# Kernel tuning notes

Measured on AMD Instinct MI355X. Metric: run time of the kernel, lower is better.

Reference implementation:

```python
import jax, jax.numpy as jnp
import numpy as np

D_MODEL = 512
N_HEADS = 8
D_FF = 1024
LV = 2048
LT = 512
GAMMA = 0.9
SCALE_BASE = 512  # XPOS default scale_base


def _dup_interleave(m):
    # (L, d/2) -> (L, d) duplicating each column: [a,b] -> [a,a,b,b]
    return jnp.repeat(m, 2, axis=-1)


def _xpos(x, downscale=False):
    # XPOS rotary embedding (RetNet-style), x: (B, L, d)
    B, L, d = x.shape
    half = d // 2
    s = (jnp.arange(0, d, 2, dtype=jnp.float32) + 0.4 * d) / (1.4 * d)  # (d/2,)
    scale = s[None, :] ** (jnp.arange(L, dtype=jnp.float32)[:, None] / SCALE_BASE)  # (L, d/2)
    inv_freq = 1.0 / (10000.0 ** (jnp.arange(half, dtype=jnp.float32) / half))
    ang = jnp.arange(L, dtype=jnp.float32)[:, None] * inv_freq[None, :]  # (L, d/2)
    if downscale:
        scale = 1.0 / scale
    sin = _dup_interleave(jnp.sin(ang) * scale)[None]  # (1, L, d)
    cos = _dup_interleave(jnp.cos(ang) * scale)[None]
    x1, x2 = x[..., 0::2], x[..., 1::2]
    rot = jnp.stack((-x2, x1), axis=-1).reshape(x.shape)  # rotate_every_two
    return x * cos + rot * sin


def _sine_pos(L, d):
    # DETR-style normalized 1D sine position embedding, mask = ones(1, L)
    x_embed = jnp.arange(1, L + 1, dtype=jnp.float32)  # cumsum of ones
    x_embed = x_embed / (x_embed[-1] + 1e-6) * (2.0 * np.pi)
    dim_t = jnp.arange(d, dtype=jnp.float32)
    dim_t = 10000.0 ** (2.0 * jnp.floor(dim_t / 2.0) / d)
    pos = x_embed[:, None] / dim_t[None, :]  # (L, d)
    pos = jnp.stack((jnp.sin(pos[:, 0::2]), jnp.cos(pos[:, 1::2])), axis=2).reshape(L, d)
    return pos[None]  # (1, L, d)


def _ln(x, w, b, eps=1e-5):
    mu = jnp.mean(x, axis=-1, keepdims=True)
    var = jnp.var(x, axis=-1, keepdims=True)
    return (x - mu) / jnp.sqrt(var + eps) * w + b


def _ret_forward(src_vid, src_txt, ln1_w, ln1_b, wq, bq, wk, bk, wv, bv, wo, bo,
                 lin1_w, lin1_b, lin2_w, lin2_b, ln2_w, ln2_b, ln3_w, ln3_b,
                 learn_ret_w):
    B, Lv, D = src_vid.shape
    Lt = src_txt.shape[1]
    h, dk = N_HEADS, D // N_HEADS

    # retention decay matrix D[n,m] = gamma^(n-m) for n>=m else 0
    n = jnp.arange(Lv)
    delta = jnp.maximum(n[:, None] - n[None, :], 0).astype(jnp.float32)
    Dm = jnp.where(n[:, None] >= n[None, :], GAMMA ** delta, 0.0)

    # learned sparse mask
    learn = jax.nn.sigmoid(learn_ret_w.reshape(Lv, Lv))
    diag = jnp.eye(Lv, dtype=jnp.float32)
    video_ret = (1.0 - diag) * learn
    learn_mask = diag + video_ret
    mask = Dm * learn_mask  # mask_choice == 'both'
    loss_sparsity = jnp.mean(jnp.abs(video_ret))

    # position encodings
    pos_vid_q = _xpos(src_vid)
    pos_vid_k = _xpos(src_vid, downscale=True)
    pos_txt = _sine_pos(Lt, D)
    src = jnp.concatenate([src_vid, src_txt], axis=1)       # (B, Lv+Lt, D)
    pos = jnp.concatenate([pos_vid_q, pos_txt], axis=1)
    pos_k = jnp.concatenate([pos_vid_k, pos_txt], axis=1)

    # --- RetLayer (eval mode: dropout = identity) ---
    src2 = _ln(src, ln1_w, ln1_b)
    q = src2[:, :Lv] + pos[:, :Lv]
    k = src2[:, :Lv] + pos_k[:, :Lv]
    v = src2[:, :Lv]

    # multi-head attention with MULTIPLICATIVE mask on logits
    qh = (q @ wq.T + bq).reshape(B, Lv, h, dk) / jnp.sqrt(jnp.float32(dk))
    kh = (k @ wk.T + bk).reshape(B, Lv, h, dk)
    vh = (v @ wv.T + bv).reshape(B, Lv, h, dk)
    attn = jnp.einsum('blhd,bmhd->bhlm', qh, kh) * mask[None, None]
    attn = jax.nn.softmax(attn, axis=-1)
    vid_att = jnp.einsum('bhlm,bmhd->blhd', attn, vh).reshape(B, Lv, D)
    vid_att = vid_att @ wo.T + bo

    src2 = jnp.concatenate([vid_att, src2[:, Lv:]], axis=1) + pos
    src = src + src2
    src2 = _ln(src, ln2_w, ln2_b)
    src2 = jax.nn.gelu(src2 @ lin1_w.T + lin1_b, approximate=False) @ lin2_w.T + lin2_b
    src = src + src2
    src = _ln(src, ln3_w, ln3_b)
    return src[:, :Lv], src[:, Lv:], loss_sparsity


def setup_inputs() -> dict:
    key = jax.random.key(0)
    ks = jax.random.split(key, 12)
    D, F = D_MODEL, D_FF
    w = lambda k, shp: (jax.random.normal(k, shp, dtype=jnp.float32) * 0.02)
    return {
        'src_vid': jax.random.normal(ks[0], (1, LV, D), dtype=jnp.float32),
        'src_txt': jax.random.normal(ks[1], (1, LT, D), dtype=jnp.float32),
        'ln1_w': jnp.ones((D,), jnp.float32), 'ln1_b': jnp.zeros((D,), jnp.float32),
        'wq': w(ks[2], (D, D)), 'bq': jnp.zeros((D,), jnp.float32),
        'wk': w(ks[3], (D, D)), 'bk': jnp.zeros((D,), jnp.float32),
        'wv': w(ks[4], (D, D)), 'bv': jnp.zeros((D,), jnp.float32),
        'wo': w(ks[5], (D, D)), 'bo': jnp.zeros((D,), jnp.float32),
        'lin1_w': w(ks[6], (F, D)), 'lin1_b': jnp.zeros((F,), jnp.float32),
        'lin2_w': w(ks[7], (D, F)), 'lin2_b': jnp.zeros((D,), jnp.float32),
        'ln2_w': jnp.ones((D,), jnp.float32), 'ln2_b': jnp.zeros((D,), jnp.float32),
        'ln3_w': jnp.ones((D,), jnp.float32), 'ln3_b': jnp.zeros((D,), jnp.float32),
        'learn_ret_w': jax.random.normal(ks[8], (LV * LV,), dtype=jnp.float32),
    }


def reference(src_vid, src_txt, ln1_w, ln1_b, wq, bq, wk, bk, wv, bv, wo, bo,
              lin1_w, lin1_b, lin2_w, lin2_b, ln2_w, ln2_b, ln3_w, ln3_b,
              learn_ret_w):
    return _ret_forward(src_vid, src_txt, ln1_w, ln1_b, wq, bq, wk, bk, wv, bv,
                        wo, bo, lin1_w, lin1_b, lin2_w, lin2_b, ln2_w, ln2_b,
                        ln3_w, ln3_b, learn_ret_w)
```

## Files before the change

### kernel.cpp

```cpp
#include <hip/hip_runtime.h>
#include <hip/hip_bf16.h>
#include <math.h>

#define LVID 2048
#define LTXT 512
#define DMOD 512
#define LTOT 2560
#define LOG2_GAMMA (-0.15200309344504995f)
#define LOG2E 1.4426950408889634f

typedef __bf16 bf16x8 __attribute__((ext_vector_type(8)));
typedef float f32x4 __attribute__((ext_vector_type(4)));

__device__ inline f32x4 mfma_bf16(bf16x8 a, bf16x8 b, f32x4 c) {
  return __builtin_amdgcn_mfma_f32_16x16x32_bf16(a, b, c, 0, 0, 0);
}

__device__ inline void gload_lds16(const void* g, void* l) {
  __builtin_amdgcn_global_load_lds(
      (const __attribute__((address_space(1))) void*)g,
      (__attribute__((address_space(3))) void*)l, 16, 0, 0);
}

union U8 { __hip_bfloat16 b[8]; uint4 u; };

__global__ __launch_bounds__(256) void k_prep_ln1(
    const float* __restrict__ lw, float* __restrict__ premask2,
    float* __restrict__ lossp,
    const float* __restrict__ wq, const float* __restrict__ wk,
    const float* __restrict__ wv, const float* __restrict__ wo,
    const float* __restrict__ l1, const float* __restrict__ l2,
    __hip_bfloat16* __restrict__ dst,
    const float* __restrict__ src_vid, const float* __restrict__ src_txt,
    const float* __restrict__ w, const float* __restrict__ b,
    __hip_bfloat16* __restrict__ acat, float* __restrict__ srcA,
    float* __restrict__ posb) {
  int tid = threadIdx.x;
  int blk = blockIdx.x;
  if (blk < 2048) {
    __shared__ float red[256];
    int idx0 = (blk * 256 + tid) * 8;
    int i = idx0 >> 11, j0 = idx0 & 2047;
    float4 lv0 = *(const float4*)&lw[idx0];
    float4 lv1 = *(const float4*)&lw[idx0 + 4];
    float lvv[8] = {lv0.x, lv0.y, lv0.z, lv0.w, lv1.x, lv1.y, lv1.z, lv1.w};
    float pm[8];
    float s = 0.f;
#pragma unroll
    for (int e = 0; e < 8; e++) {
      int j = j0 + e;
      float sig = 1.f / (1.f + __expf(-lvv[e]));
      if (j != i) s += sig;
      float m = (j > i) ? 0.f
              : ((j == i) ? 1.f : exp2f((float)(i - j) * LOG2_GAMMA) * sig);
      pm[e] = m * LOG2E;
    }
    *(float4*)&premask2[idx0]     = *(float4*)&pm[0];
    *(float4*)&premask2[idx0 + 4] = *(float4*)&pm[4];
    red[tid] = s; __syncthreads();
    for (int st = 128; st > 0; st >>= 1) { if (tid < st) red[tid] += red[tid + st]; __syncthreads(); }
    if (tid == 0) lossp[blk] = red[0];
  } else if (blk < 4096) {
    int i4 = (blk - 2048) * 256 + tid;
    const float* sp; int base;
    if (i4 < 131072)      { if (i4 < 65536)  { sp = wq; base = 0; }      else { sp = wk; base = 65536; } }
    else if (i4 < 262144) { if (i4 < 196608) { sp = wv; base = 131072; } else { sp = wo; base = 196608; } }
    else if (i4 < 393216) { sp = l1; base = 262144; }
    else                  { sp = l2; base = 393216; }
    float4 v = ((const float4*)sp)[i4 - base];
    __hip_bfloat16 o[4] = {__float2bfloat16(v.x), __float2bfloat16(v.y),
                           __float2bfloat16(v.z), __float2bfloat16(v.w)};
    *(uint2*)(dst + (size_t)i4 * 4) = *(uint2*)o;
  } else {
    int row = (blk - 4096) * 4 + (tid >> 6);
    int lane = tid & 63;
    const float* xs = (row < LVID) ? (src_vid + (size_t)row * DMOD)
                                   : (src_txt + (size_t)(row - LVID) * DMOD);
    float x[8];
    { float4 v0 = *(const float4*)&xs[lane * 8];
      float4 v1 = *(const float4*)&xs[lane * 8 + 4];
      x[0]=v0.x; x[1]=v0.y; x[2]=v0.z; x[3]=v0.w;
      x[4]=v1.x; x[5]=v1.y; x[6]=v1.z; x[7]=v1.w; }
    float s = 0.f;
#pragma unroll
    for (int i = 0; i < 8; i++) s += x[i];
#pragma unroll
    for (int st = 1; st < 64; st <<= 1) s += __shfl_xor(s, st, 64);
    float mu = s * (1.f / DMOD);
    float vs = 0.f;
#pragma unroll
    for (int i = 0; i < 8; i++) { float d = x[i] - mu; vs += d * d; }
#pragma unroll
    for (int st = 1; st < 64; st <<= 1) vs += __shfl_xor(vs, st, 64);
    float inv = rsqrtf(vs * (1.f / DMOD) + 1e-5f);
    float y[8];
    { float4 w0 = *(const float4*)&w[lane * 8];
      float4 w1 = *(const float4*)&w[lane * 8 + 4];
      float4 b0 = *(const float4*)&b[lane * 8];
      float4 b1 = *(const float4*)&b[lane * 8 + 4];
      float wv_[8] = {w0.x,w0.y,w0.z,w0.w,w1.x,w1.y,w1.z,w1.w};
      float bv_[8] = {b0.x,b0.y,b0.z,b0.w,b1.x,b1.y,b1.z,b1.w};
#pragma unroll
      for (int i = 0; i < 8; i++) y[i] = (x[i] - mu) * inv * wv_[i] + bv_[i]; }
    size_t base = (size_t)row * DMOD + lane * 8;
    if (row < LVID) {
      U8 pv;
#pragma unroll
      for (int i = 0; i < 8; i++) pv.b[i] = __float2bfloat16(y[i]);
      *(uint4*)&acat[(size_t)(4096 + row) * DMOD + lane * 8] = pv.u;
      float pq[8], pk[8];
      float l = (float)row;
#pragma unroll
      for (int p = 0; p < 4; p++) {
        int j = lane * 4 + p;
        float sj = (2.f * j + 204.8f) * (1.f / 716.8f);
        float scale = __powf(sj, l * (1.f / 512.f));
        float invfreq = __powf(10000.f, -(float)j * (1.f / 256.f));
        float sn, cs; __sincosf(l * invfreq, &sn, &cs);
        float cq = cs * scale, sq = sn * scale;
        pq[2*p]   = x[2*p] * cq - x[2*p+1] * sq;
        pq[2*p+1] = x[2*p+1] * cq + x[2*p] * sq;
        float isc = 1.f / scale;
        float ck = cs * isc, sk = sn * isc;
        pk[2*p]   = x[2*p] * ck - x[2*p+1] * sk;
        pk[2*p+1] = x[2*p+1] * ck + x[2*p] * sk;
      }
      *(float4*)&posb[base]     = *(float4*)&pq[0];
      *(float4*)&posb[base + 4] = *(float4*)&pq[4];
      U8 pqv, pkv;
#pragma unroll
      for (int i = 0; i < 8; i++) {
        pqv.b[i] = __float2bfloat16(y[i] + pq[i]);
        pkv.b[i] = __float2bfloat16(y[i] + pk[i]);
      }
      *(uint4*)&acat[(size_t)row * DMOD + lane * 8] = pqv.u;
      *(uint4*)&acat[(size_t)(2048 + row) * DMOD + lane * 8] = pkv.u;
    } else {
      int l = row - LVID;
      float xe = (float)(l + 1) * (6.28318530717958647692f / 512.000001f);
      float o8[8];
#pragma unroll
      for (int p = 0; p < 4; p++) {
        int j = lane * 4 + p;
        float dimt = __powf(10000.f, (float)j * (1.f / 256.f));
        float a = xe / dimt;
        o8[2*p]   = x[2*p]   + y[2*p]   + __sinf(a);
        o8[2*p+1] = x[2*p+1] + y[2*p+1] + __cosf(a);
      }
      *(float4*)&srcA[base]     = *(float4*)&o8[0];
      *(float4*)&srcA[base + 4] = *(float4*)&o8[4];
    }
  }
}

__global__ __launch_bounds__(256) void k_ln2(
    const float* __restrict__ srcA,
    const float* __restrict__ w, const float* __restrict__ b,
    __hip_bfloat16* __restrict__ obf) {
  int row = blockIdx.x * 4 + (threadIdx.x >> 6);
  int lane = threadIdx.x & 63;
  size_t base = (size_t)row * DMOD + lane * 8;
  float x[8];
  { float4 v0 = *(const float4*)&srcA[base];
    float4 v1 = *(const float4*)&srcA[base + 4];
    x[0]=v0.x; x[1]=v0.y; x[2]=v0.z; x[3]=v0.w;
    x[4]=v1.x; x[5]=v1.y; x[6]=v1.z; x[7]=v1.w; }
  float s = 0.f;
#pragma unroll
  for (int i = 0; i < 8; i++) s += x[i];
#pragma unroll
  for (int st = 1; st < 64; st <<= 1) s += __shfl_xor(s, st, 64);
  float mu = s * (1.f / DMOD);
  float vs = 0.f;
#pragma unroll
  for (int i = 0; i < 8; i++) { float d = x[i] - mu; vs += d * d; }
#pragma unroll
  for (int st = 1; st < 64; st <<= 1) vs += __shfl_xor(vs, st, 64);
  float inv = rsqrtf(vs * (1.f / DMOD) + 1e-5f);
  float4 w0 = *(const float4*)&w[lane * 8];
  float4 w1 = *(const float4*)&w[lane * 8 + 4];
  float4 b0 = *(const float4*)&b[lane * 8];
  float4 b1 = *(const float4*)&b[lane * 8 + 4];
  float wv_[8] = {w0.x,w0.y,w0.z,w0.w,w1.x,w1.y,w1.z,w1.w};
  float bv_[8] = {b0.x,b0.y,b0.z,b0.w,b1.x,b1.y,b1.z,b1.w};
  U8 o;
#pragma unroll
  for (int i = 0; i < 8; i++)
    o.b[i] = __float2bfloat16((x[i] - mu) * inv * wv_[i] + bv_[i]);
  *(uint4*)&obf[base] = o.u;
}

__global__ __launch_bounds__(256) void k_ln3(
    const float* __restrict__ srcA, const float* __restrict__ ffo,
    const float* __restrict__ w, const float* __restrict__ b,
    float* __restrict__ o, const float* __restrict__ lossp) {
  if (blockIdx.x == 0 && threadIdx.x < 64) {
    float s = 0.f;
    for (int i = threadIdx.x; i < 2048; i += 64) s += lossp[i];
#pragma unroll
    for (int st = 1; st < 64; st <<= 1) s += __shfl_xor(s, st, 64);
    if (threadIdx.x == 0) o[1310720] = s * (1.f / 4194304.f);
  }
  int row = blockIdx.x * 4 + (threadIdx.x >> 6);
  int lane = threadIdx.x & 63;
  size_t base = (size_t)row * DMOD + lane * 8;
  float x[8];
  { float4 a0 = *(const float4*)&srcA[base];
    float4 a1 = *(const float4*)&srcA[base + 4];
    float4 f0 = *(const float4*)&ffo[base];
    float4 f1 = *(const float4*)&ffo[base + 4];
    x[0]=a0.x+f0.x; x[1]=a0.y+f0.y; x[2]=a0.z+f0.z; x[3]=a0.w+f0.w;
    x[4]=a1.x+f1.x; x[5]=a1.y+f1.y; x[6]=a1.z+f1.z; x[7]=a1.w+f1.w; }
  float s = 0.f;
#pragma unroll
  for (int i = 0; i < 8; i++) s += x[i];
#pragma unroll
  for (int st = 1; st < 64; st <<= 1) s += __shfl_xor(s, st, 64);
  float mu = s * (1.f / DMOD);
  float vs = 0.f;
#pragma unroll
  for (int i = 0; i < 8; i++) { float d = x[i] - mu; vs += d * d; }
#pragma unroll
  for (int st = 1; st < 64; st <<= 1) vs += __shfl_xor(vs, st, 64);
  float inv = rsqrtf(vs * (1.f / DMOD) + 1e-5f);
  float4 w0 = *(const float4*)&w[lane * 8];
  float4 w1 = *(const float4*)&w[lane * 8 + 4];
  float4 b0 = *(const float4*)&b[lane * 8];
  float4 b1 = *(const float4*)&b[lane * 8 + 4];
  float wv_[8] = {w0.x,w0.y,w0.z,w0.w,w1.x,w1.y,w1.z,w1.w};
  float bv_[8] = {b0.x,b0.y,b0.z,b0.w,b1.x,b1.y,b1.z,b1.w};
  float y[8];
#pragma unroll
  for (int i = 0; i < 8; i++) y[i] = (x[i] - mu) * inv * wv_[i] + bv_[i];
  *(float4*)&o[base]     = *(float4*)&y[0];
  *(float4*)&o[base + 4] = *(float4*)&y[4];
}

template <int EPI>
__global__ __launch_bounds__(256) void k_gemm3(
    const __hip_bfloat16* __restrict__ A, const __hip_bfloat16* __restrict__ W0,
    const float* __restrict__ b0, const float* __restrict__ b1,
    const float* __restrict__ b2, void* __restrict__ Cv,
    const float* __restrict__ res1, const float* __restrict__ res2,
    float* __restrict__ vtot, int M, int N, int K) {
  __shared__ __hip_bfloat16 sA[2][4096];
  __shared__ __hip_bfloat16 sB[2][4096];
  int tid = threadIdx.x, lane = tid & 63, w = tid >> 6;
  int c16 = lane & 15, q4 = lane >> 4;
  int bm = blockIdx.y * 128, bn = blockIdx.x * 128;
  int seg = (EPI == 3) ? (bm >> 11) : 0;
  const __hip_bfloat16* Wp = (EPI == 3) ? (W0 + (size_t)seg * ((size_t)N * K)) : W0;
  int r0 = tid >> 2, cc0 = (tid & 3) * 8;
  const __hip_bfloat16* gA0 = A  + (size_t)(bm + r0) * K + cc0;
  const __hip_bfloat16* gA1 = A  + (size_t)(bm + 64 + r0) * K + cc0;
  const __hip_bfloat16* gB0 = Wp + (size_t)(bn + r0) * K + cc0;
  const __hip_bfloat16* gB1 = Wp + (size_t)(bn + 64 + r0) * K + cc0;
  auto stage = [&](int buf, int k0) {
    gload_lds16(gA0 + k0, &sA[buf][(size_t)tid * 8]);
    gload_lds16(gA1 + k0, &sA[buf][2048 + (size_t)tid * 8]);
    gload_lds16(gB0 + k0, &sB[buf][(size_t)tid * 8]);
    gload_lds16(gB1 + k0, &sB[buf][2048 + (size_t)tid * 8]);
  };
  f32x4 acc[4][4];
  { f32x4 z = {0.f,0.f,0.f,0.f};
#pragma unroll
    for (int i = 0; i < 4; i++)
#pragma unroll
      for (int j = 0; j < 4; j++) acc[i][j] = z; }
  int wm = w & 1, wn = w >> 1;
  const int S = K >> 5;
  stage(0, 0);
  for (int s = 0; s < S; s++) {
    __syncthreads();
    if (s + 1 < S) stage((s + 1) & 1, (s + 1) * 32);
    int bf = s & 1;
    bf16x8 af[4], bfr[4];
#pragma unroll
    for (int i = 0; i < 4; i++)
      af[i] = *(const bf16x8*)&sA[bf][(wm*64 + i*16 + c16) * 32 + q4*8];
#pragma unroll
    for (int j = 0; j < 4; j++)
      bfr[j] = *(const bf16x8*)&sB[bf][(wn*64 + j*16 + c16) * 32 + q4*8];
#pragma unroll
    for (int i = 0; i < 4; i++)
#pragma unroll
      for (int j = 0; j < 4; j++)
        acc[i][j] = mfma_bf16(af[i], bfr[j], acc[i][j]);
  }
  float alpha = (EPI == 3 && seg == 0) ? 0.125f : 1.f;
  const float* bp = (EPI == 3) ? (seg == 0 ? b0 : (seg == 1 ? b1 : b2)) : b0;
  float vsum[4] = {0.f, 0.f, 0.f, 0.f};
#pragma unroll
  for (int j = 0; j < 4; j++) {
    int n = bn + wn*64 + j*16 + c16;
    float bs = bp[n];
#pragma unroll
    for (int i = 0; i < 4; i++) {
#pragma unroll
      for (int r = 0; r < 4; r++) {
        int m = bm + wm*64 + i*16 + q4*4 + r;
        float v = (acc[i][j][r] + bs) * alpha;
        if (EPI == 4) v = 0.5f * v * (1.f + erff(v * 0.70710678118654752f));
        if (EPI == 0) {
          ((float*)Cv)[(size_t)m * N + n] = v;
        } else if (EPI == 2) {
          size_t off = (size_t)m * N + n;
          ((float*)Cv)[off] = v + res1[off] + res2[off];
        } else if (EPI == 4) {
          ((__hip_bfloat16*)Cv)[(size_t)m * N + n] = __float2bfloat16(v);
        } else {
          __hip_bfloat16 vb = __float2bfloat16(v);
          ((__hip_bfloat16*)Cv)[(size_t)(m & 2047) * 1536 + seg * 512 + n] = vb;
          if (seg == 2) vsum[j] += __bfloat162float(vb);
        }
      }
    }
  }
  if (EPI == 3 && seg == 2) {
#pragma unroll
    for (int j = 0; j < 4; j++) {
      float s2 = vsum[j];
      s2 += __shfl_xor(s2, 16, 64);
      s2 += __shfl_xor(s2, 32, 64);
      if (q4 == 0) atomicAdd(&vtot[bn + wn*64 + j*16 + c16], s2);
    }
  }
}

__global__ __launch_bounds__(256) void k_attn(
    const __hip_bfloat16* __restrict__ qkv,
    const float* __restrict__ premask2,
    const float* __restrict__ Vtot,
    __hip_bfloat16* __restrict__ outp) {
  __shared__ __hip_bfloat16 sQ[64][72];
  __shared__ __hip_bfloat16 sK[2][64][72];
  __shared__ __hip_bfloat16 sVt[2][64][72];
  __shared__ __hip_bfloat16 sP[64][72];
  __shared__ float sVa[4][64];
  int i0 = blockIdx.x * 64, h = blockIdx.y;
  int tid = threadIdx.x, lane = tid & 63, w = tid >> 6;
  int c16 = lane & 15, q4 = lane >> 4;
  {
    int r = tid >> 2, c0 = (tid & 3) * 16;
    const __hip_bfloat16* g = qkv + (size_t)(i0 + r) * 1536 + h * 64 + c0;
    *(uint4*)&sQ[r][c0]     = *(const uint4*)g;
    *(uint4*)&sQ[r][c0 + 8] = *(const uint4*)(g + 8);
  }
  int thi = i0 >> 6;
  int tlo = (i0 > 900) ? ((i0 - 900) >> 6) : 0;
  float rm = 0.f, rz = 0.f;
  f32x4 O[4];
  { f32x4 z = {0.f,0.f,0.f,0.f}; O[0]=z; O[1]=z; O[2]=z; O[3]=z; }
  float vacc = 0.f;
  int kr = tid >> 2, kc = (tid & 3) * 16;
  uint4 pk0, pk1;
  U8 pv0, pv1;
  {
    const __hip_bfloat16* gk = qkv + (size_t)(tlo*64 + kr) * 1536 + 512 + h*64 + kc;
    pk0 = *(const uint4*)gk; pk1 = *(const uint4*)(gk + 8);
    const __hip_bfloat16* gv = qkv + (size_t)(tlo*64 + w*16) * 1536 + 1024 + h*64 + lane;
#pragma unroll
    for (int j = 0; j < 8; j++) pv0.b[j] = gv[(size_t)j * 1536];
#pragma unroll
    for (int j = 0; j < 8; j++) pv1.b[j] = gv[(size_t)(j + 8) * 1536];
  }
  for (int t = tlo; t <= thi; t++) {
    int buf = (t - tlo) & 1;
    *(uint4*)&sK[buf][kr][kc]       = pk0;
    *(uint4*)&sK[buf][kr][kc + 8]   = pk1;
    *(uint4*)&sVt[buf][lane][w*16]     = pv0.u;
    *(uint4*)&sVt[buf][lane][w*16 + 8] = pv1.u;
#pragma unroll
    for (int j = 0; j < 8; j++) vacc += __bfloat162float(pv0.b[j]);
#pragma unroll
    for (int j = 0; j < 8; j++) vacc += __bfloat162float(pv1.b[j]);
    __syncthreads();
    if (t < thi) {
      const __hip_bfloat16* gk = qkv + (size_t)((t+1)*64 + kr) * 1536 + 512 + h*64 + kc;
      pk0 = *(const uint4*)gk; pk1 = *(const uint4*)(gk + 8);
      const __hip_bfloat16* gv = qkv + (size_t)((t+1)*64 + w*16) * 1536 + 1024 + h*64 + lane;
#pragma unroll
      for (int j = 0; j < 8; j++) pv0.b[j] = gv[(size_t)j * 1536];
#pragma unroll
      for (int j = 0; j < 8; j++) pv1.b[j] = gv[(size_t)(j + 8) * 1536];
    }
    bf16x8 bq0 = *(const bf16x8*)&sQ[w*16 + c16][q4*8];
    bf16x8 bq1 = *(const bf16x8*)&sQ[w*16 + c16][32 + q4*8];
    f32x4 St[4];
#pragma unroll
    for (int jt = 0; jt < 4; jt++) {
      f32x4 z = {0.f,0.f,0.f,0.f};
      bf16x8 a0 = *(const bf16x8*)&sK[buf][jt*16 + c16][q4*8];
      bf16x8 a1 = *(const bf16x8*)&sK[buf][jt*16 + c16][32 + q4*8];
      z = mfma_bf16(a0, bq0, z);
      z = mfma_bf16(a1, bq1, z);
      St[jt] = z;
    }
    int qg = i0 + w*16 + c16;
    float lg[4][4];
    float tmax = -3.0e38f;
#pragma unroll
    for (int jt = 0; jt < 4; jt++) {
      float4 pm = *(const float4*)&premask2[(size_t)qg * 2048 + t*64 + jt*16 + q4*4];
      lg[jt][0] = St[jt][0] * pm.x; lg[jt][1] = St[jt][1] * pm.y;
      lg[jt][2] = St[jt][2] * pm.z; lg[jt][3] = St[jt][3] * pm.w;
#pragma unroll
      for (int r = 0; r < 4; r++) tmax = fmaxf(tmax, lg[jt][r]);
    }
    tmax = fmaxf(tmax, __shfl_xor(tmax, 16, 64));
    tmax = fmaxf(tmax, __shfl_xor(tmax, 32, 64));
    float mn = fmaxf(rm, tmax);
    float al = exp2f(rm - mn);
    rm = mn;
    float zp = 0.f;
#pragma unroll
    for (int jt = 0; jt < 4; jt++) {
      U8 e4;
      float e0 = exp2f(lg[jt][0] - rm), e1 = exp2f(lg[jt][1] - rm);
      float e2 = exp2f(lg[jt][2] - rm), e3 = exp2f(lg[jt][3] - rm);
      zp += e0 + e1 + e2 + e3;
      e4.b[0] = __float2bfloat16(e0); e4.b[1] = __float2bfloat16(e1);
      e4.b[2] = __float2bfloat16(e2); e4.b[3] = __float2bfloat16(e3);
      *(uint2*)&sP[w*16 + c16][jt*16 + q4*4] = *(uint2*)&e4.b[0];
    }
    zp += __shfl_xor(zp, 16, 64);
    zp += __shfl_xor(zp, 32, 64);
    rz = rz * al + zp;
    float alr[4];
#pragma unroll
    for (int r = 0; r < 4; r++) alr[r] = __shfl(al, q4*4 + r, 64);
#pragma unroll
    for (int dt = 0; dt < 4; dt++)
#pragma unroll
      for (int r = 0; r < 4; r++) O[dt][r] *= alr[r];
    bf16x8 ap0 = *(const bf16x8*)&sP[w*16 + c16][q4*8];
    bf16x8 ap1 = *(const bf16x8*)&sP[w*16 + c16][32 + q4*8];
#pragma unroll
    for (int dt = 0; dt < 4; dt++) {
      bf16x8 bv0 = *(const bf16x8*)&sVt[buf][dt*16 + c16][q4*8];
      bf16x8 bv1 = *(const bf16x8*)&sVt[buf][dt*16 + c16][32 + q4*8];
      O[dt] = mfma_bf16(ap0, bv0, O[dt]);
      O[dt] = mfma_bf16(ap1, bv1, O[dt]);
    }
  }
  sVa[w][lane] = vacc;
  __syncthreads();
  float rmr[4], rzr[4];
#pragma unroll
  for (int r = 0; r < 4; r++) {
    rmr[r] = __shfl(rm, q4*4 + r, 64);
    rzr[r] = __shfl(rz, q4*4 + r, 64);
  }
  float nu = (float)(2048 - 64 * (thi - tlo + 1));
#pragma unroll
  for (int dt = 0; dt < 4; dt++) {
    int d = dt*16 + c16;
    float va = sVa[0][d] + sVa[1][d] + sVa[2][d] + sVa[3][d];
    float vu = Vtot[h*64 + d] - va;
#pragma unroll
    for (int r = 0; r < 4; r++) {
      float eu = exp2f(-rmr[r]);
      float o = (O[dt][r] + eu * vu) / (rzr[r] + nu * eu);
      outp[(size_t)(i0 + w*16 + q4*4 + r) * DMOD + h*64 + d] = __float2bfloat16(o);
    }
  }
}

extern "C" void kernel_launch(void* const* d_in, const int* in_sizes, int n_in,
                              void* d_out, int out_size, void* d_ws, size_t ws_size,
                              hipStream_t stream) {
  const float* src_vid = (const float*)d_in[0];
  const float* src_txt = (const float*)d_in[1];
  const float* ln1_w = (const float*)d_in[2];
  const float* ln1_b = (const float*)d_in[3];
  const float* wq = (const float*)d_in[4];
  const float* bq = (const float*)d_in[5];
  const float* wk = (const float*)d_in[6];
  const float* bk = (const float*)d_in[7];
  const float* wv = (const float*)d_in[8];
  const float* bv = (const float*)d_in[9];
  const float* wo = (const float*)d_in[10];
  const float* bo = (const float*)d_in[11];
  const float* lin1_w = (const float*)d_in[12];
  const float* lin1_b = (const float*)d_in[13];
  const float* lin2_w = (const float*)d_in[14];
  const float* lin2_b = (const float*)d_in[15];
  const float* ln2_w = (const float*)d_in[16];
  const float* ln2_b = (const float*)d_in[17];
  const float* ln3_w = (const float*)d_in[18];
  const float* ln3_b = (const float*)d_in[19];
  const float* lw = (const float*)d_in[20];
  float* out = (float*)d_out;

  char* wsb = (char*)d_ws;
  float* premask2       = (float*)(wsb + 0);
  __hip_bfloat16* wqb   = (__hip_bfloat16*)(wsb + 16777216);
  __hip_bfloat16* wob   = wqb + 786432;
  __hip_bfloat16* l1b   = wqb + 1048576;
  __hip_bfloat16* l2b   = wqb + 1572864;
  __hip_bfloat16* acat  = (__hip_bfloat16*)(wsb + 20971520);
  __hip_bfloat16* qkvb  = (__hip_bfloat16*)(wsb + 27262976);
  __hip_bfloat16* vattb = (__hip_bfloat16*)(wsb + 33554432);
  float* srcA           = (float*)(wsb + 35651584);
  float* posb           = (float*)(wsb + 46137344);
  __hip_bfloat16* s2b   = (__hip_bfloat16*)(wsb + 51380224);
  __hip_bfloat16* hidb  = (__hip_bfloat16*)(wsb + 54525952);
  float* ffo            = (float*)(wsb + 59768832);
  float* Vtot           = (float*)(wsb + 65011712);
  float* lossp          = Vtot + 512;

  hipMemsetAsync(Vtot, 0, 512 * sizeof(float), stream);

  k_prep_ln1<<<4736, 256, 0, stream>>>(lw, premask2, lossp,
      wq, wk, wv, wo, lin1_w, lin2_w, wqb,
      src_vid, src_txt, ln1_w, ln1_b, acat, srcA, posb);

  k_gemm3<3><<<dim3(4, 48), 256, 0, stream>>>(acat, wqb, bq, bk, bv,
      qkvb, nullptr, nullptr, Vtot, 6144, 512, 512);
  k_attn<<<dim3(32, 8), 256, 0, stream>>>(qkvb, premask2, Vtot, vattb);
  k_gemm3<2><<<dim3(4, 16), 256, 0, stream>>>(vattb, wob, bo, nullptr, nullptr,
      srcA, src_vid, posb, nullptr, 2048, 512, 512);
  k_ln2<<<640, 256, 0, stream>>>(srcA, ln2_w, ln2_b, s2b);
  k_gemm3<4><<<dim3(8, 20), 256, 0, stream>>>(s2b, l1b, lin1_b, nullptr, nullptr,
      hidb, nullptr, nullptr, nullptr, 2560, 1024, 512);
  k_gemm3<0><<<dim3(4, 20), 256, 0, stream>>>(hidb, l2b, lin2_b, nullptr, nullptr,
      ffo, nullptr, nullptr, nullptr, 2560, 512, 1024);
  k_ln3<<<640, 256, 0, stream>>>(srcA, ffo, ln3_w, ln3_b, out, lossp);
}
```

Before: 245.7 us.

## Shrink GEMM tiles to 64x64 and split-K the second FFN GEMM

Every GEMM now uses 64x64 block tiles instead of 128x128, giving four times as many workgroups so the small matrices fill more of the GPU's compute units. The lin2 GEMM is also split along K into two halves that write separate fp32 partial buffers, and the LN3 kernel sums them. The cost is less data reuse per tile, more global and LDS traffic per flop, and an extra fp32 buffer that LN3 must read.

```diff
diff --git a/kernel.cpp b/kernel.cpp
--- a/kernel.cpp
+++ b/kernel.cpp
@@ -191,7 +191,8 @@
 }
 
 __global__ __launch_bounds__(256) void k_ln3(
-    const float* __restrict__ srcA, const float* __restrict__ ffo,
+    const float* __restrict__ srcA, const float* __restrict__ ffo0,
+    const float* __restrict__ ffo1,
     const float* __restrict__ w, const float* __restrict__ b,
     float* __restrict__ o, const float* __restrict__ lossp) {
   if (blockIdx.x == 0 && threadIdx.x < 64) {
@@ -207,10 +208,12 @@
   float x[8];
   { float4 a0 = *(const float4*)&srcA[base];
     float4 a1 = *(const float4*)&srcA[base + 4];
-    float4 f0 = *(const float4*)&ffo[base];
-    float4 f1 = *(const float4*)&ffo[base + 4];
-    x[0]=a0.x+f0.x; x[1]=a0.y+f0.y; x[2]=a0.z+f0.z; x[3]=a0.w+f0.w;
-    x[4]=a1.x+f1.x; x[5]=a1.y+f1.y; x[6]=a1.z+f1.z; x[7]=a1.w+f1.w; }
+    float4 f0 = *(const float4*)&ffo0[base];
+    float4 f1 = *(const float4*)&ffo0[base + 4];
+    float4 g0 = *(const float4*)&ffo1[base];
+    float4 g1 = *(const float4*)&ffo1[base + 4];
+    x[0]=a0.x+f0.x+g0.x; x[1]=a0.y+f0.y+g0.y; x[2]=a0.z+f0.z+g0.z; x[3]=a0.w+f0.w+g0.w;
+    x[4]=a1.x+f1.x+g1.x; x[5]=a1.y+f1.y+g1.y; x[6]=a1.z+f1.z+g1.z; x[7]=a1.w+f1.w+g1.w; }
   float s = 0.f;
 #pragma unroll
   for (int i = 0; i < 8; i++) s += x[i];
@@ -237,77 +240,69 @@
 }
 
 template <int EPI>
-__global__ __launch_bounds__(256) void k_gemm3(
+__global__ __launch_bounds__(256) void k_gemm4(
     const __hip_bfloat16* __restrict__ A, const __hip_bfloat16* __restrict__ W0,
     const float* __restrict__ b0, const float* __restrict__ b1,
     const float* __restrict__ b2, void* __restrict__ Cv,
     const float* __restrict__ res1, const float* __restrict__ res2,
     float* __restrict__ vtot, int M, int N, int K) {
-  __shared__ __hip_bfloat16 sA[2][4096];
-  __shared__ __hip_bfloat16 sB[2][4096];
+  __shared__ __hip_bfloat16 sA[2][2048];
+  __shared__ __hip_bfloat16 sB[2][2048];
   int tid = threadIdx.x, lane = tid & 63, w = tid >> 6;
   int c16 = lane & 15, q4 = lane >> 4;
-  int bm = blockIdx.y * 128, bn = blockIdx.x * 128;
+  int bm = blockIdx.y * 64, bn = blockIdx.x * 64;
   int seg = (EPI == 3) ? (bm >> 11) : 0;
   const __hip_bfloat16* Wp = (EPI == 3) ? (W0 + (size_t)seg * ((size_t)N * K)) : W0;
+  int kb   = (EPI == 5) ? (int)blockIdx.z * (K >> 1) : 0;
+  int Keff = (EPI == 5) ? (K >> 1) : K;
   int r0 = tid >> 2, cc0 = (tid & 3) * 8;
-  const __hip_bfloat16* gA0 = A  + (size_t)(bm + r0) * K + cc0;
-  const __hip_bfloat16* gA1 = A  + (size_t)(bm + 64 + r0) * K + cc0;
-  const __hip_bfloat16* gB0 = Wp + (size_t)(bn + r0) * K + cc0;
-  const __hip_bfloat16* gB1 = Wp + (size_t)(bn + 64 + r0) * K + cc0;
+  const __hip_bfloat16* gA = A  + (size_t)(bm + r0) * K + kb + cc0;
+  const __hip_bfloat16* gB = Wp + (size_t)(bn + r0) * K + kb + cc0;
   auto stage = [&](int buf, int k0) {
-    gload_lds16(gA0 + k0, &sA[buf][(size_t)tid * 8]);
-    gload_lds16(gA1 + k0, &sA[buf][2048 + (size_t)tid * 8]);
-    gload_lds16(gB0 + k0, &sB[buf][(size_t)tid * 8]);
-    gload_lds16(gB1 + k0, &sB[buf][2048 + (size_t)tid * 8]);
+    gload_lds16(gA + k0, &sA[buf][(size_t)tid * 8]);
+    gload_lds16(gB + k0, &sB[buf][(size_t)tid * 8]);
   };
-  f32x4 acc[4][4];
-  { f32x4 z = {0.f,0.f,0.f,0.f};
-#pragma unroll
-    for (int i = 0; i < 4; i++)
-#pragma unroll
-      for (int j = 0; j < 4; j++) acc[i][j] = z; }
+  f32x4 acc[2][2];
+  { f32x4 z = {0.f,0.f,0.f,0.f}; acc[0][0]=z; acc[0][1]=z; acc[1][0]=z; acc[1][1]=z; }
   int wm = w & 1, wn = w >> 1;
-  const int S = K >> 5;
+  const int S = Keff >> 5;
   stage(0, 0);
   for (int s = 0; s < S; s++) {
     __syncthreads();
     if (s + 1 < S) stage((s + 1) & 1, (s + 1) * 32);
     int bf = s & 1;
-    bf16x8 af[4], bfr[4];
-#pragma unroll
-    for (int i = 0; i < 4; i++)
-      af[i] = *(const bf16x8*)&sA[bf][(wm*64 + i*16 + c16) * 32 + q4*8];
-#pragma unroll
-    for (int j = 0; j < 4; j++)
-      bfr[j] = *(const bf16x8*)&sB[bf][(wn*64 + j*16 + c16) * 32 + q4*8];
-#pragma unroll
-    for (int i = 0; i < 4; i++)
-#pragma unroll
-      for (int j = 0; j < 4; j++)
-        acc[i][j] = mfma_bf16(af[i], bfr[j], acc[i][j]);
+    bf16x8 af[2], bfr[2];
+    af[0]  = *(const bf16x8*)&sA[bf][(wm*32 + c16) * 32 + q4*8];
+    af[1]  = *(const bf16x8*)&sA[bf][(wm*32 + 16 + c16) * 32 + q4*8];
+    bfr[0] = *(const bf16x8*)&sB[bf][(wn*32 + c16) * 32 + q4*8];
+    bfr[1] = *(const bf16x8*)&sB[bf][(wn*32 + 16 + c16) * 32 + q4*8];
+    acc[0][0] = mfma_bf16(af[0], bfr[0], acc[0][0]);
+    acc[0][1] = mfma_bf16(af[0], bfr[1], acc[0][1]);
+    acc[1][0] = mfma_bf16(af[1], bfr[0], acc[1][0]);
+    acc[1][1] = mfma_bf16(af[1], bfr[1], acc[1][1]);
   }
   float alpha = (EPI == 3 && seg == 0) ? 0.125f : 1.f;
   const float* bp = (EPI == 3) ? (seg == 0 ? b0 : (seg == 1 ? b1 : b2)) : b0;
-  float vsum[4] = {0.f, 0.f, 0.f, 0.f};
-#pragma unroll
-  for (int j = 0; j < 4; j++) {
-    int n = bn + wn*64 + j*16 + c16;
+  float vsum[2] = {0.f, 0.f};
+#pragma unroll
+  for (int j = 0; j < 2; j++) {
+    int n = bn + wn*32 + j*16 + c16;
     float bs = bp[n];
-#pragma unroll
-    for (int i = 0; i < 4; i++) {
+    if (EPI == 5 && blockIdx.z != 0) bs = 0.f;
+#pragma unroll
+    for (int i = 0; i < 2; i++) {
 #pragma unroll
       for (int r = 0; r < 4; r++) {
-        int m = bm + wm*64 + i*16 + q4*4 + r;
+        int m = bm + wm*32 + i*16 + q4*4 + r;
         float v = (acc[i][j][r] + bs) * alpha;
         if (EPI == 4) v = 0.5f * v * (1.f + erff(v * 0.70710678118654752f));
-        if (EPI == 0) {
-          ((float*)Cv)[(size_t)m * N + n] = v;
-        } else if (EPI == 2) {
+        if (EPI == 2) {
           size_t off = (size_t)m * N + n;
           ((float*)Cv)[off] = v + res1[off] + res2[off];
         } else if (EPI == 4) {
           ((__hip_bfloat16*)Cv)[(size_t)m * N + n] = __float2bfloat16(v);
+        } else if (EPI == 5) {
+          ((float*)Cv)[(size_t)blockIdx.z * 1310720 + (size_t)m * N + n] = v;
         } else {
           __hip_bfloat16 vb = __float2bfloat16(v);
           ((__hip_bfloat16*)Cv)[(size_t)(m & 2047) * 1536 + seg * 512 + n] = vb;
@@ -318,11 +313,11 @@
   }
   if (EPI == 3 && seg == 2) {
 #pragma unroll
-    for (int j = 0; j < 4; j++) {
+    for (int j = 0; j < 2; j++) {
       float s2 = vsum[j];
       s2 += __shfl_xor(s2, 16, 64);
       s2 += __shfl_xor(s2, 32, 64);
-      if (q4 == 0) atomicAdd(&vtot[bn + wn*64 + j*16 + c16], s2);
+      if (q4 == 0) atomicAdd(&vtot[bn + wn*32 + j*16 + c16], s2);
     }
   }
 }
@@ -505,8 +500,9 @@
   float* posb           = (float*)(wsb + 46137344);
   __hip_bfloat16* s2b   = (__hip_bfloat16*)(wsb + 51380224);
   __hip_bfloat16* hidb  = (__hip_bfloat16*)(wsb + 54525952);
-  float* ffo            = (float*)(wsb + 59768832);
-  float* Vtot           = (float*)(wsb + 65011712);
+  float* ffo0           = (float*)(wsb + 59768832);
+  float* ffo1           = (float*)(wsb + 65011712);
+  float* Vtot           = (float*)(wsb + 70254592);
   float* lossp          = Vtot + 512;
 
   hipMemsetAsync(Vtot, 0, 512 * sizeof(float), stream);
@@ -515,15 +511,15 @@
       wq, wk, wv, wo, lin1_w, lin2_w, wqb,
       src_vid, src_txt, ln1_w, ln1_b, acat, srcA, posb);
 
-  k_gemm3<3><<<dim3(4, 48), 256, 0, stream>>>(acat, wqb, bq, bk, bv,
+  k_gemm4<3><<<dim3(8, 96), 256, 0, stream>>>(acat, wqb, bq, bk, bv,
       qkvb, nullptr, nullptr, Vtot, 6144, 512, 512);
   k_attn<<<dim3(32, 8), 256, 0, stream>>>(qkvb, premask2, Vtot, vattb);
-  k_gemm3<2><<<dim3(4, 16), 256, 0, stream>>>(vattb, wob, bo, nullptr, nullptr,
+  k_gemm4<2><<<dim3(8, 32), 256, 0, stream>>>(vattb, wob, bo, nullptr, nullptr,
       srcA, src_vid, posb, nullptr, 2048, 512, 512);
   k_ln2<<<640, 256, 0, stream>>>(srcA, ln2_w, ln2_b, s2b);
-  k_gemm3<4><<<dim3(8, 20), 256, 0, stream>>>(s2b, l1b, lin1_b, nullptr, nullptr,
+  k_gemm4<4><<<dim3(16, 40), 256, 0, stream>>>(s2b, l1b, lin1_b, nullptr, nullptr,
       hidb, nullptr, nullptr, nullptr, 2560, 1024, 512);
-  k_gemm3<0><<<dim3(4, 20), 256, 0, stream>>>(hidb, l2b, lin2_b, nullptr, nullptr,
-      ffo, nullptr, nullptr, nullptr, 2560, 512, 1024);
-  k_ln3<<<640, 256, 0, stream>>>(srcA, ffo, ln3_w, ln3_b, out, lossp);
-}
+  k_gemm4<5><<<dim3(8, 40, 2), 256, 0, stream>>>(hidb, l2b, lin2_b, nullptr, nullptr,
+      ffo0, nullptr, nullptr, nullptr, 2560, 512, 1024);
+  k_ln3<<<640, 256, 0, stream>>>(srcA, ffo0, ffo1, ln3_w, ln3_b, out, lossp);
+}
```

Measured after the change: 221.2 us. 10.0% less time.
